# Kernel tuning notes

Measured on AMD Instinct MI355X. Metric: run time of the kernel, lower is better.

Reference implementation:

```python
import jax, jax.numpy as jnp
import numpy as np

T = 2048; H = 1024; NH = 16; NKV = 4; HD = 64
E = 32; TOPK = 4; NG = 4; TG = 2; IM = 384; ISH = 384
ROT = HD // 2          # partial_rotary_factor = 0.5
EPS = 1e-5; RSF = 1.0; THETA = 10000.0


def setup_inputs() -> dict:
    ks = jax.random.split(jax.random.key(0), 12)
    g = lambda k, sh, sc=0.02: jax.random.normal(k, sh, jnp.float32) * sc
    return {
        "hidden_states": g(ks[0], (T, H), 1.0),
        "residual": g(ks[1], (T, H), 1.0),
        "in_ln_w": jnp.ones((H,), jnp.float32),
        "post_ln_w": jnp.ones((H,), jnp.float32),
        "q_norm_w": jnp.ones((HD,), jnp.float32),
        "k_norm_w": jnp.ones((HD,), jnp.float32),
        "Wqkv": g(ks[2], (H, (NH + 2 * NKV) * HD)),
        "Wo": g(ks[3], (NH * HD, H)),
        "Wg": g(ks[4], (H, E)),
        "gate_bias": g(ks[5], (E,), 0.1),
        "Wgu": g(ks[6], (E, H, 2 * IM)),
        "Wd": g(ks[7], (E, IM, H)),
        "Wgu_sh": g(ks[8], (H, 2 * ISH)),
        "Wd_sh": g(ks[9], (ISH, H)),
        "positions": jnp.arange(T, dtype=jnp.int32),
    }


def _rms(x, w):
    return x * jax.lax.rsqrt(jnp.mean(x * x, -1, keepdims=True) + EPS) * w


def _rope(x, pos):
    # neox-style rotary on the first ROT dims of each head; x: [T, nheads, HD]
    half = ROT // 2
    inv = THETA ** (-(jnp.arange(half, dtype=jnp.float32) * 2.0 / ROT))
    ang = pos.astype(jnp.float32)[:, None] * inv          # [T, half]
    c = jnp.cos(ang)[:, None, :]
    s = jnp.sin(ang)[:, None, :]
    x1, x2, rest = x[..., :half], x[..., half:ROT], x[..., ROT:]
    return jnp.concatenate([x1 * c - x2 * s, x1 * s + x2 * c, rest], -1)


def _layer(pos, hidden, residual, in_ln_w, post_ln_w, q_norm_w, k_norm_w,
           Wqkv, Wo, Wg, gate_bias, Wgu, Wd, Wgu_sh, Wd_sh):
    # fused add-RMSNorm (vllm RMSNorm(x, residual))
    residual = hidden + residual
    hidden = _rms(residual, in_ln_w)

    # self-attention (GQA, per-head qk-norm, partial rotary, causal)
    qkv = hidden @ Wqkv
    q = qkv[:, :NH * HD].reshape(T, NH, HD)
    k = qkv[:, NH * HD:(NH + NKV) * HD].reshape(T, NKV, HD)
    v = qkv[:, (NH + NKV) * HD:].reshape(T, NKV, HD)
    q = _rms(q, q_norm_w)
    k = _rms(k, k_norm_w)
    q = _rope(q, pos)
    k = _rope(k, pos)
    rep = NH // NKV
    k = jnp.repeat(k, rep, axis=1)
    v = jnp.repeat(v, rep, axis=1)
    scores = jnp.einsum('thd,shd->hts', q, k) * (HD ** -0.5)
    causal = pos[:, None] >= pos[None, :]
    scores = jnp.where(causal[None], scores, -jnp.inf)
    attn = jax.nn.softmax(scores, axis=-1)
    o = jnp.einsum('hts,shd->thd', attn, v).reshape(T, NH * HD)
    hidden = o @ Wo

    # post-attention fused add-RMSNorm
    residual = hidden + residual
    hidden = _rms(residual, post_ln_w)

    # --- Glm4MoE: grouped sigmoid top-k router with e_score_correction_bias ---
    logits = hidden.astype(jnp.float32) @ Wg            # gate runs in fp32
    scr = jax.nn.sigmoid(logits)                        # [T, E]
    sfc = scr + gate_bias                               # scores_for_choice
    # group score = sum of top-2 biased scores within each group
    gs = jnp.sum(jax.lax.top_k(sfc.reshape(T, NG, E // NG), 2)[0], -1)  # [T, NG]
    _, gidx = jax.lax.top_k(gs, TG)
    gmask = jnp.zeros((T, NG), jnp.float32).at[jnp.arange(T)[:, None], gidx].set(1.0)
    emask = jnp.repeat(gmask, E // NG, axis=1)          # [T, E]
    _, ids = jax.lax.top_k(jnp.where(emask > 0, sfc, -jnp.inf), TOPK)
    w = jnp.take_along_axis(scr, ids, axis=1)           # weights from unbiased scores
    w = w / jnp.sum(w, -1, keepdims=True)               # renormalize (norm_topk_prob)
    wdense = jnp.zeros((T, E), jnp.float32).at[jnp.arange(T)[:, None], ids].set(w)

    # routed experts: dense-over-experts reference for the grouped GEMM dispatch
    gu = jnp.einsum('th,ehi->tei', hidden, Wgu)         # [T, E, 2*IM]
    act = jax.nn.silu(gu[..., :IM]) * gu[..., IM:]      # SiluAndMul
    routed = jnp.einsum('te,tei,eih->th', wdense, act, Wd)

    # shared expert MLP
    gus = hidden @ Wgu_sh
    shared = (jax.nn.silu(gus[:, :ISH]) * gus[:, ISH:]) @ Wd_sh

    hidden = routed * RSF + shared
    return hidden, residual


def reference(hidden_states, residual, in_ln_w, post_ln_w, q_norm_w, k_norm_w,
              Wqkv, Wo, Wg, gate_bias, Wgu, Wd, Wgu_sh, Wd_sh, positions):
    return _layer(positions, hidden_states, residual, in_ln_w, post_ln_w,
                  q_norm_w, k_norm_w, Wqkv, Wo, Wg, gate_bias, Wgu, Wd,
                  Wgu_sh, Wd_sh)
```

## Files before the change

### kernel.cpp

```cpp
#include <hip/hip_runtime.h>
#include <math.h>

#define TT 2048
#define HH 1024
#define NHEADS 16
#define NKVH 4
#define HDIM 64
#define NEXP 32
#define TOPK_ 4
#define NGRP 4
#define IMID 384
#define ISHARED 384
#define QKV_W (24*64)
#define EPS_ 1e-5f
#define MAXSB 288
#define NSPLITS 80

typedef __attribute__((ext_vector_type(8))) short short8;
typedef __attribute__((ext_vector_type(4))) float f32x4;

__device__ __forceinline__ ushort f2bf(float x) {
  union { float f; unsigned u; } v; v.f = x;
  unsigned r = v.u + 0x7fffu + ((v.u >> 16) & 1u);
  return (ushort)(r >> 16);
// ... 12 lines not shown
  return *(const short8*)(As + ((lg * 32 + (row ^ lg)) * 8));
}
__device__ __forceinline__ short8 read_a_frag64(const ushort* As, int lg, int row) {
  return *(const short8*)(As + ((lg * 64 + (row ^ lg)) * 8));
}
__device__ __forceinline__ short8 read_b_frag(const ushort* Bs, int lg, int col) {
  int boff = (col * 16) ^ (((col >> 3) & 7) << 4);
  return *(const short8*)((const char*)Bs + lg * 1024 + boff);
}

__device__ __forceinline__ void stage_B_tile(const float* __restrict__ B, int ldb,
                                             int k0, int col0, ushort* Bs, int tid) {
  int a = tid >> 4;
  int cG = tid & 15;
  int k = 2 * a;
  const float* p0 = B + (size_t)(k0 + k) * ldb + col0 + cG * 4;
  const float* p1 = p0 + ldb;
  float4 r0 = *(const float4*)p0;
  float4 r1 = *(const float4*)p1;
  int gg = (k & 15) >> 2;
  int slot = (k & 3) + ((k >> 4) << 2);
  float v0[4] = {r0.x, r0.y, r0.z, r0.w};
  float v1[4] = {r1.x, r1.y, r1.z, r1.w};
  char* plane = (char*)Bs + gg * 1024;
  #pragma unroll
  for (int j = 0; j < 4; ++j) {
    int c = cG * 4 + j;
    unsigned pk = (unsigned)f2bf(v0[j]) | ((unsigned)f2bf(v1[j]) << 16);
    int boff = ((c * 16) ^ (((c >> 3) & 7) << 4)) + slot * 2;
    *(unsigned*)(plane + boff) = pk;
  }
}

__global__ __launch_bounds__(256) void pack_B_kernel(
    const float* __restrict__ src, ushort* __restrict__ dst, int N) {
  __shared__ ushort tileB[2048];
  int tid = threadIdx.x;
  stage_B_tile(src, N, blockIdx.y * 32, blockIdx.x * 64, tileB, tid);
  __syncthreads();
  size_t toff = ((size_t)blockIdx.y * gridDim.x + blockIdx.x) * 2048;
  *(short8*)(dst + toff + tid * 8) = *(const short8*)(tileB + tid * 8);
}

__global__ __launch_bounds__(256) void gemm64_bb(
    const ushort* __restrict__ Ab, const ushort* __restrict__ Bpk,
    float* __restrict__ C, int M, int N, int K) {
  __shared__ ushort As[4][2048];
  __shared__ ushort Bs[4][2048];
  int tid = threadIdx.x;
  int row0 = blockIdx.y * 64, col0 = blockIdx.x * 64;
  int ntn = N >> 6;
  int wid = tid >> 6, lane = tid & 63;
  int lg = lane >> 4, lr = lane & 15;
  int wrow = (wid >> 1) * 32, wcol = (wid & 1) * 32;
  const ushort* asrc = Ab + (size_t)(row0 + (lane ^ wid)) * K + wid * 8;
  const ushort* bsrc = Bpk + (size_t)blockIdx.x * 2048 + wid * 512 + lane * 8;
  const int NT = K >> 5;
  f32x4 acc[2][2] = {};

  auto issue = [&](int tt) {
    int b = tt & 3;
    gload16(asrc + tt * 32, &As[b][wid * 512]);
    gload16(bsrc + (size_t)tt * ntn * 2048, &Bs[b][wid * 512]);
  };
  issue(0); issue(1); issue(2);
  for (int t = 0; t < NT; ++t) {
    int ahead = NT - 1 - t;
    if (ahead >= 2)      asm volatile("s_waitcnt vmcnt(4)" ::: "memory");
    else if (ahead == 1) asm volatile("s_waitcnt vmcnt(2)" ::: "memory");
    else                 asm volatile("s_waitcnt vmcnt(0)" ::: "memory");
    __builtin_amdgcn_s_barrier();
    if (t + 3 < NT) issue(t + 3);
    int cb = t & 3;
    short8 af0 = read_a_frag64(&As[cb][0], lg, wrow + lr);
    short8 af1 = read_a_frag64(&As[cb][0], lg, wrow + 16 + lr);
    #pragma unroll
    for (int nn = 0; nn < 2; ++nn) {
      short8 bf_ = read_b_frag(&Bs[cb][0], lg, wcol + nn * 16 + lr);
      acc[0][nn] = __builtin_amdgcn_mfma_f32_16x16x32_bf16(af0, bf_, acc[0][nn], 0, 0, 0);
      acc[1][nn] = __builtin_amdgcn_mfma_f32_16x16x32_bf16(af1, bf_, acc[1][nn], 0, 0, 0);
    }
  }
  #pragma unroll
  for (int mm = 0; mm < 2; ++mm)
    #pragma unroll
    for (int nn = 0; nn < 2; ++nn) {
      int row = row0 + wrow + mm * 16 + lg * 4;
      int col = col0 + wcol + nn * 16 + lr;
      #pragma unroll
      for (int i = 0; i < 4; ++i)
        C[(size_t)(row + i) * N + col] = acc[mm][nn][i];
    }
}

__global__ __launch_bounds__(256) void moe_up_pk(
    const ushort* __restrict__ hln2b, const ushort* __restrict__ Wpk,
    const int* __restrict__ perm, const int* __restrict__ offs,
    const int* __restrict__ counts, const int* __restrict__ sb_e,
    const int* __restrict__ sb_base, const int* __restrict__ nsb,
    ushort* __restrict__ actb) {
  int b = blockIdx.x;
  int sb = ((b & 7) * 36) + (b >> 3);
  if (sb >= *nsb) return;
  int e = sb_e[sb];
  int base = sb_base[sb];
  int start = offs[e];
  int nt = min(32, counts[e] - base);
  int tid = threadIdx.x;
  int wid = tid >> 6, lane = tid & 63;
  int lg = lane >> 4, lr = lane & 15;
  int bz = blockIdx.y * 2 + (wid >> 1);
  int wcol = (wid & 1) * 32;
  int tok0 = perm[start + base + min(lr, nt - 1)] >> 2;
  int tok1 = perm[start + base + min(16 + lr, nt - 1)] >> 2;
  const ushort* a0p = hln2b + (size_t)tok0 * HH + lg * 8;
  const ushort* a1p = hln2b + (size_t)tok1 * HH + lg * 8;
  int c0 = wcol + lr, c1 = wcol + 16 + lr;
  int sw0 = (c0 * 16) ^ (((c0 >> 3) & 7) << 4);
  int sw1 = (c1 * 16) ^ (((c1 >> 3) & 7) << 4);
  const char* gbase = (const char*)Wpk + ((size_t)(e * 32) * 12 + bz) * 4096 + lg * 1024;
  const char* ubase = gbase + (size_t)6 * 4096;
  const size_t bstep = (size_t)12 * 4096;
  f32x4 accg[2][2] = {}, accu[2][2] = {};
  short8 a0c = *(const short8*)(a0p);
  short8 a1c = *(const short8*)(a1p);
  short8 g0c = *(const short8*)(gbase + sw0);
  short8 g1c = *(const short8*)(gbase + sw1);
  short8 u0c = *(const short8*)(ubase + sw0);
  short8 u1c = *(const short8*)(ubase + sw1);
  #pragma unroll 4
  for (int t = 0; t < 31; ++t) {
    const char* gb = gbase + (size_t)(t + 1) * bstep;
    const char* ub = ubase + (size_t)(t + 1) * bstep;
    short8 a0n = *(const short8*)(a0p + (t + 1) * 32);
    short8 a1n = *(const short8*)(a1p + (t + 1) * 32);
    short8 g0n = *(const short8*)(gb + sw0);
    short8 g1n = *(const short8*)(gb + sw1);
    short8 u0n = *(const short8*)(ub + sw0);
    short8 u1n = *(const short8*)(ub + sw1);
    accg[0][0] = __builtin_amdgcn_mfma_f32_16x16x32_bf16(a0c, g0c, accg[0][0], 0, 0, 0);
    accg[0][1] = __builtin_amdgcn_mfma_f32_16x16x32_bf16(a0c, g1c, accg[0][1], 0, 0, 0);
    accg[1][0] = __builtin_amdgcn_mfma_f32_16x16x32_bf16(a1c, g0c, accg[1][0], 0, 0, 0);
    accg[1][1] = __builtin_amdgcn_mfma_f32_16x16x32_bf16(a1c, g1c, accg[1][1], 0, 0, 0);
    accu[0][0] = __builtin_amdgcn_mfma_f32_16x16x32_bf16(a0c, u0c, accu[0][0], 0, 0, 0);
    accu[0][1] = __builtin_amdgcn_mfma_f32_16x16x32_bf16(a0c, u1c, accu[0][1], 0, 0, 0);
    accu[1][0] = __builtin_amdgcn_mfma_f32_16x16x32_bf16(a1c, u0c, accu[1][0], 0, 0, 0);
    accu[1][1] = __builtin_amdgcn_mfma_f32_16x16x32_bf16(a1c, u1c, accu[1][1], 0, 0, 0);
    a0c = a0n; a1c = a1n; g0c = g0n; g1c = g1n; u0c = u0n; u1c = u1n;
  }
  accg[0][0] = __builtin_amdgcn_mfma_f32_16x16x32_bf16(a0c, g0c, accg[0][0], 0, 0, 0);
  accg[0][1] = __builtin_amdgcn_mfma_f32_16x16x32_bf16(a0c, g1c, accg[0][1], 0, 0, 0);
  accg[1][0] = __builtin_amdgcn_mfma_f32_16x16x32_bf16(a1c, g0c, accg[1][0], 0, 0, 0);
  accg[1][1] = __builtin_amdgcn_mfma_f32_16x16x32_bf16(a1c, g1c, accg[1][1], 0, 0, 0);
  accu[0][0] = __builtin_amdgcn_mfma_f32_16x16x32_bf16(a0c, u0c, accu[0][0], 0, 0, 0);
  accu[0][1] = __builtin_amdgcn_mfma_f32_16x16x32_bf16(a0c, u1c, accu[0][1], 0, 0, 0);
  accu[1][0] = __builtin_amdgcn_mfma_f32_16x16x32_bf16(a1c, u0c, accu[1][0], 0, 0, 0);
  accu[1][1] = __builtin_amdgcn_mfma_f32_16x16x32_bf16(a1c, u1c, accu[1][1], 0, 0, 0);
  #pragma unroll
  for (int mm = 0; mm < 2; ++mm)
    #pragma unroll
    for (int nn = 0; nn < 2; ++nn) {
      int pcol = bz * 64 + wcol + ((lr >> 2) << 3) + (nn << 2) + (lr & 3);
      #pragma unroll
      for (int i = 0; i < 4; ++i) {
        int rr = mm * 16 + lg * 4 + i;
        if (rr < nt) {
          float gv = accg[mm][nn][i], uv = accu[mm][nn][i];
          float av = gv / (1.f + expf(-gv)) * uv;
          actb[(size_t)(start + base + rr) * IMID + pcol] = f2bf(av);
        }
      }
    }
}

__global__ __launch_bounds__(256) void moe_down_pk(
    const ushort* __restrict__ actb, const ushort* __restrict__ Wpk,
    const int* __restrict__ offs, const int* __restrict__ counts,
    const int* __restrict__ sb_e, const int* __restrict__ sb_base,
    const int* __restrict__ nsb, ushort* __restrict__ partialb) {
  int b = blockIdx.x;
  int sb = ((b & 7) * 36) + (b >> 3);
  if (sb >= *nsb) return;
  int e = sb_e[sb];
  int base = sb_base[sb];
  int start = offs[e];
  int nt = min(32, counts[e] - base);
  __shared__ ushort As[3][1024];
  __shared__ ushort Bs[3][2048];
  int tid = threadIdx.x;
  int bz = blockIdx.y, col0 = bz * 64;
  int wid = tid >> 6, lane = tid & 63;
  int lg = lane >> 4, lr = lane & 15;
  int wrow = (wid >> 1) * 16, wcol = (wid & 1) * 32;
  const ushort* bt0 = Wpk + ((size_t)(e * 12) * 16 + bz) * 2048 + wid * 512 + lane * 8;
  int ga = wid * 2 + (lane >> 5);
  const ushort* asrcA = actb + (size_t)(start + base + ((lane & 31) ^ ga)) * IMID + ga * 8;
  const int NT = IMID >> 5;
  f32x4 acc[2] = {};

  auto issue = [&](int tt) {
    int bb = tt % 3;
    if (wid < 2) gload16(asrcA + tt * 32, &As[bb][wid * 512]);
    gload16(bt0 + (size_t)tt * 16 * 2048, &Bs[bb][wid * 512]);
  };
  issue(0); issue(1);
  for (int t = 0; t < NT; ++t) {
    if (t < NT - 1) {
      if (wid < 2) asm volatile("s_waitcnt vmcnt(2)" ::: "memory");
      else         asm volatile("s_waitcnt vmcnt(1)" ::: "memory");
    } else {
      asm volatile("s_waitcnt vmcnt(0)" ::: "memory");
    }
    __builtin_amdgcn_s_barrier();
    if (t + 2 < NT) issue(t + 2);
    int cb = t % 3;
    short8 af = read_a_frag32(&As[cb][0], lg, wrow + lr);
    #pragma unroll
    for (int nn = 0; nn < 2; ++nn) {
      short8 bf_ = read_b_frag(&Bs[cb][0], lg, wcol + nn * 16 + lr);
      acc[nn] = __builtin_amdgcn_mfma_f32_16x16x32_bf16(af, bf_, acc[nn], 0, 0, 0);
    }
  }
  #pragma unroll
  for (int nn = 0; nn < 2; ++nn)
    #pragma unroll
    for (int i = 0; i < 4; ++i) {
      int rr = wrow + lg * 4 + i;
      if (rr < nt)
        partialb[(size_t)(start + base + rr) * HH + col0 + wcol + nn * 16 + lr] = f2bf(acc[nn][i]);
    }
}

__global__ __launch_bounds__(256) void add_rms_kernel(
    const float* __restrict__ a, const float* __restrict__ b,
    const float* __restrict__ w, float* __restrict__ sum_out,
    float* __restrict__ ln_out, ushort* __restrict__ lnb) {
  int t = blockIdx.x, tid = threadIdx.x;
  float4 x = reinterpret_cast<const float4*>(a + (size_t)t*HH)[tid];
  float4 y = reinterpret_cast<const float4*>(b + (size_t)t*HH)[tid];
  x.x += y.x; x.y += y.y; x.z += y.z; x.w += y.w;
  float ss = x.x*x.x + x.y*x.y + x.z*x.z + x.w*x.w;
  #pragma unroll
  for (int off = 1; off < 64; off <<= 1) ss += __shfl_xor(ss, off);
  __shared__ float wsum[4];
  int wid = tid >> 6, lane = tid & 63;
  if (lane == 0) wsum[wid] = ss;
  __syncthreads();
  float tot = wsum[0] + wsum[1] + wsum[2] + wsum[3];
  float r = rsqrtf(tot * (1.0f/HH) + EPS_);
  reinterpret_cast<float4*>(sum_out + (size_t)t*HH)[tid] = x;
  float4 wl = reinterpret_cast<const float4*>(w)[tid];
  float4 o = make_float4(x.x*r*wl.x, x.y*r*wl.y, x.z*r*wl.z, x.w*r*wl.w);
  reinterpret_cast<float4*>(ln_out + (size_t)t*HH)[tid] = o;
  ushort4 ub;
  ub.x = f2bf(o.x); ub.y = f2bf(o.y); ub.z = f2bf(o.z); ub.w = f2bf(o.w);
  int dst = ((tid >> 3) << 5) + ((tid & 3) << 3) + (((tid >> 2) & 1) << 2);
  *(ushort4*)(lnb + (size_t)t * HH + dst) = ub;
}

__global__ __launch_bounds__(256) void qk_norm_rope_kernel(
    float* __restrict__ qkv, const float* __restrict__ qw,
    const float* __restrict__ kw, const int* __restrict__ pos) {
  int t = blockIdx.x;
  int hh = blockIdx.y * 4 + (threadIdx.x >> 6);
  int lane = threadIdx.x & 63;
  float* p = qkv + (size_t)t * QKV_W + hh * HDIM;
  float x = p[lane];
  float ss = x * x;
  #pragma unroll
  for (int off = 1; off < 64; off <<= 1) ss += __shfl_xor(ss, off);
  float r = rsqrtf(ss * (1.0f/HDIM) + EPS_);
  float wv = (hh < NHEADS ? qw : kw)[lane];
  float xn = x * r * wv;
  float partner = __shfl_xor(xn, 16);
  float out = xn;
  if (lane < 32) {
    int i = lane & 15;
    float inv = powf(10000.0f, -(float)i / 16.0f);
    float ang = (float)pos[t] * inv;
    float cv = cosf(ang), sv = sinf(ang);
    out = (lane < 16) ? (xn * cv - partner * sv) : (partner * sv + xn * cv);
  }
  p[lane] = out;
}

__global__ __launch_bounds__(256) void pack_KV_kernel(
    const float* __restrict__ qkv, ushort* __restrict__ Kpk,
    ushort* __restrict__ Vpk) {
  __shared__ ushort kimg[2048];
  __shared__ ushort vimg[2048];
  int tid = threadIdx.x;
  int kt = blockIdx.x, kvh = blockIdx.y;
  {
    int c = tid >> 7, t2 = tid & 127;
    int g = t2 & 3, r = t2 >> 2;
    const float* kp = qkv + (size_t)(kt*32 + r) * QKV_W + NHEADS*HDIM + kvh*HDIM + 32*c + 4*g;
    float4 h0 = *(const float4*)kp;
    float4 h1 = *(const float4*)(kp + 16);
    short8 v;
    v[0]=(short)f2bf(h0.x); v[1]=(short)f2bf(h0.y); v[2]=(short)f2bf(h0.z); v[3]=(short)f2bf(h0.w);
    v[4]=(short)f2bf(h1.x); v[5]=(short)f2bf(h1.y); v[6]=(short)f2bf(h1.z); v[7]=(short)f2bf(h1.w);
    *(short8*)(kimg + c*1024 + (g*32 + (r^g))*8) = v;
  }
  stage_B_tile(qkv + (size_t)(NHEADS+NKVH)*HDIM + (size_t)kvh*HDIM, QKV_W, kt*32, 0, vimg, tid);
  __syncthreads();
  size_t toff = ((size_t)(kvh * (TT/32) + kt)) * 2048;
  *(short8*)(Kpk + toff + tid * 8) = *(const short8*)(kimg + tid * 8);
  *(short8*)(Vpk + toff + tid * 8) = *(const short8*)(vimg + tid * 8);
}

__global__ __launch_bounds__(256) void attn_v3_kernel(
    const float* __restrict__ qkv, const ushort* __restrict__ Kpk,
    const ushort* __restrict__ Vpk, ushort* __restrict__ ob,
    float* __restrict__ po, float* __restrict__ pl) {
  __shared__ ushort Ks[3][2048];
  __shared__ ushort Vs[3][2048];
  int tid = threadIdx.x;
  int wid = tid >> 6, lane = tid & 63;
  int lg = lane >> 4, lr = lane & 15;
  int h = blockIdx.y;
  int f = blockIdx.x;
  int g = 0;
  while (f >= 4 * (g + 1) * (g + 2)) ++g;
  int r_ = f - 4 * g * (g + 1);
  int ns = g + 1;
  int qb = 8 * g + r_ / ns;
  int s = r_ % ns;
  int tiles_total = 2 * qb + 2;
  int per = (tiles_total + ns - 1) / ns;
  int lo = s * per;
  int nloc = min(per, tiles_total - lo);
  int kvh = h >> 2;
  int q0 = qb * 64 + wid * 16;
  int qg = q0 + lr;
  const float SCL = 0.125f * 1.44269504f;
  const float FM = 16.0f;

  const float* qrow = qkv + (size_t)qg * QKV_W + h * HDIM;
  short8 qfr[2];
  #pragma unroll
  for (int c = 0; c < 2; ++c) {
    float4 a = *(const float4*)(qrow + 32*c + 4*lg);
    float4 b = *(const float4*)(qrow + 32*c + 4*lg + 16);
    short8 v;
    v[0]=(short)f2bf(a.x*SCL); v[1]=(short)f2bf(a.y*SCL); v[2]=(short)f2bf(a.z*SCL); v[3]=(short)f2bf(a.w*SCL);
    v[4]=(short)f2bf(b.x*SCL); v[5]=(short)f2bf(b.y*SCL); v[6]=(short)f2bf(b.z*SCL); v[7]=(short)f2bf(b.w*SCL);
    qfr[c] = v;
  }

  const ushort* ksrc = Kpk + (size_t)(kvh * (TT/32) + lo) * 2048 + wid * 512 + lane * 8;
  const ushort* vsrc = Vpk + (size_t)(kvh * (TT/32) + lo) * 2048 + wid * 512 + lane * 8;

  f32x4 o_acc[4] = {};
  float l_st = 0.f;
// ... 53 lines not shown
    short8 pa = pu.s8;
    #pragma unroll
    for (int nd = 0; nd < 4; ++nd) {
      short8 vf = read_b_frag(&Vs[cb][0], lg, 16*nd + lr);
      o_acc[nd] = __builtin_amdgcn_mfma_f32_16x16x32_bf16(pa, vf, o_acc[nd], 0, 0, 0);
    }
  }

  if (ns == 1) {
    #pragma unroll
    for (int i = 0; i < 4; ++i) {
      float lrow = __shfl(l_st, 4*lg + i);
      float inv = 1.0f / lrow;
      int row = q0 + 4*lg + i;
      ushort* op = ob + (size_t)row * (NHEADS*HDIM) + h * HDIM;
      #pragma unroll
      for (int nd = 0; nd < 4; ++nd) {
        int pcol = ((nd >> 1) << 5) + ((lr >> 2) << 3) + ((nd & 1) << 2) + (lr & 3);
        op[pcol] = f2bf(o_acc[nd][i] * inv);
      }
    }
  } else {
    float* pob = po + ((size_t)f * NHEADS + h) * 4096;
    #pragma unroll
    for (int nd = 0; nd < 4; ++nd)
      #pragma unroll
      for (int i = 0; i < 4; ++i)
        pob[(wid * 16 + lg * 4 + i) * 64 + 16 * nd + lr] = o_acc[nd][i];
    if (lg == 0)
      pl[((size_t)f * NHEADS + h) * 64 + wid * 16 + lr] = l_st;
  }
}

__global__ __launch_bounds__(256) void attn_combine_kernel(
    const float* __restrict__ po, const float* __restrict__ pl,
    ushort* __restrict__ ob) {
  int h = blockIdx.x;
  int qb = 8 + blockIdx.y;
  int g = qb >> 3;
  int ns = g + 1;
  int f0 = 4 * g * (g + 1) + (qb - 8 * g) * ns;
  int tid = threadIdx.x;
  int r = tid >> 2, c = tid & 3;
  float acc[16] = {};
  float lsum = 0.f;
  for (int s = 0; s < ns; ++s) {
    size_t base = ((size_t)(f0 + s) * NHEADS + h) * 4096 + r * 64 + c * 16;
    #pragma unroll
    for (int j = 0; j < 4; ++j) {
      float4 v = *(const float4*)(po + base + j * 4);
      acc[j*4+0] += v.x; acc[j*4+1] += v.y; acc[j*4+2] += v.z; acc[j*4+3] += v.w;
    }
    lsum += pl[((size_t)(f0 + s) * NHEADS + h) * 64 + r];
  }
  float inv = 1.0f / lsum;
  int row = qb * 64 + r;
  ushort* op = ob + (size_t)row * (NHEADS*HDIM) + h * HDIM + (c >> 1) * 32 + (c & 1) * 4;
  #pragma unroll
  for (int a = 0; a < 4; ++a) {
    ushort4 u;
    u.x = f2bf(acc[a*4+0] * inv); u.y = f2bf(acc[a*4+1] * inv);
    u.z = f2bf(acc[a*4+2] * inv); u.w = f2bf(acc[a*4+3] * inv);
    *(ushort4*)(op + a * 8) = u;
  }
}

__global__ __launch_bounds__(256) void router_kernel(
    const float* __restrict__ hln, const float* __restrict__ Wg,
    const float* __restrict__ bias, int* __restrict__ sel_e,
    float* __restrict__ sel_w) {
  __shared__ float hid[4][HH];
  int tid = threadIdx.x, wid = tid >> 6, lane = tid & 63;
  int t = blockIdx.x * 4 + wid;
  const float4* src = (const float4*)(hln + (size_t)t * HH);
  float4* dst = (float4*)hid[wid];
  #pragma unroll
  for (int j = 0; j < 4; ++j) dst[j * 64 + lane] = src[j * 64 + lane];
  int e = lane & 31, half = lane >> 5;
  const float* wp = Wg + (size_t)(half * 512) * NEXP + e;
  const float* hp = hid[wid] + half * 512;
  float p = 0.f;
  #pragma unroll 8
  for (int h = 0; h < 512; ++h) p += hp[h] * wp[(size_t)h * NEXP];
  p += __shfl_xor(p, 32);
  float sc = 1.0f / (1.0f + expf(-p));
  float sfc = sc + bias[e];
  float m1 = sfc, m2 = -1e30f;
  #pragma unroll
  for (int off = 1; off <= 4; off <<= 1) {
    float om1 = __shfl_xor(m1, off), om2 = __shfl_xor(m2, off);
    float hi_ = fmaxf(m1, om1);
    float lo_ = fmaxf(fminf(m1, om1), fmaxf(m2, om2));
    m1 = hi_; m2 = lo_;
  }
  float gs = m1 + m2;
  float gv[4] = {__shfl(gs, 0), __shfl(gs, 8), __shfl(gs, 16), __shfl(gs, 24)};
  int g1 = 0; float b1 = gv[0];
  #pragma unroll
  for (int g = 1; g < 4; ++g) if (gv[g] > b1) { b1 = gv[g]; g1 = g; }
  int g2 = -1; float b2 = -1e30f;
  #pragma unroll
  for (int g = 0; g < 4; ++g) if (g != g1 && gv[g] > b2) { b2 = gv[g]; g2 = g; }
  bool keep = ((e >> 3) == g1) || ((e >> 3) == g2);
  float cand = keep ? sfc : -1e30f;
  int ids[4]; float wv[4]; float wsum = 0.f;
  #pragma unroll
  for (int s = 0; s < 4; ++s) {
    float v = cand; int ix = e;
    #pragma unroll
    for (int off = 1; off < 64; off <<= 1) {
      float ov = __shfl_xor(v, off); int oix = __shfl_xor(ix, off);
      if (ov > v || (ov == v && oix < ix)) { v = ov; ix = oix; }
    }
    ids[s] = ix;
    if (e == ix) cand = -1e30f;
    float w = __shfl(sc, ix);
    wv[s] = w; wsum += w;
  }
  if (lane == 0) {
    #pragma unroll
    for (int s = 0; s < 4; ++s) {
      sel_e[t * 4 + s] = ids[s];
      sel_w[t * 4 + s] = wv[s] / wsum;
    }
  }
}

__global__ __launch_bounds__(256) void count_kernel(
    const int* __restrict__ sel_e, int* __restrict__ counts) {
  int e = blockIdx.x, tid = threadIdx.x;
  int c = 0;
  for (int i = tid; i < TT * TOPK_; i += 256) c += (sel_e[i] == e);
  #pragma unroll
  for (int off = 1; off < 64; off <<= 1) c += __shfl_xor(c, off);
  __shared__ int wsum[4];
  if ((tid & 63) == 0) wsum[tid >> 6] = c;
  __syncthreads();
  if (tid == 0) counts[e] = wsum[0] + wsum[1] + wsum[2] + wsum[3];
}

__global__ void scan_kernel(const int* __restrict__ counts,
                            int* __restrict__ offs, int* __restrict__ cursor,
                            int* __restrict__ sb_e, int* __restrict__ sb_base,
                            int* __restrict__ nsb) {
  if (threadIdx.x == 0) {
    int acc = 0, n = 0;
    for (int e = 0; e < NEXP; ++e) {
      offs[e] = acc; cursor[e] = acc;
      int c = counts[e];
      for (int b = 0; b < c; b += 32) { sb_e[n] = e; sb_base[n] = b; ++n; }
      acc += c;
    }
    *nsb = n;
  }
}

__global__ void scatter_kernel(const int* __restrict__ sel_e,
                               int* __restrict__ cursor, int* __restrict__ perm,
                               int* __restrict__ ipos) {
  int i = blockIdx.x * 256 + threadIdx.x;
  if (i < TT * TOPK_) {
    int e = sel_e[i];
    int pos = atomicAdd(&cursor[e], 1);
    perm[pos] = i;
    ipos[i] = pos;
  }
}

__global__ __launch_bounds__(256) void silu_shared_kernel(
    const float* __restrict__ gus, ushort* __restrict__ shsb) {
  int i = blockIdx.x * 256 + threadIdx.x;
  if (i < TT * (ISHARED/4)) {
    int t = i / (ISHARED/4), k = i % (ISHARED/4);
    const float* gp = gus + (size_t)t * (2*ISHARED) + k * 4;
    float4 g4 = *(const float4*)gp;
    float4 u4 = *(const float4*)(gp + ISHARED);
    ushort4 r;
    r.x = f2bf(g4.x / (1.f + expf(-g4.x)) * u4.x);
    r.y = f2bf(g4.y / (1.f + expf(-g4.y)) * u4.y);
    r.z = f2bf(g4.z / (1.f + expf(-g4.z)) * u4.z);
    r.w = f2bf(g4.w / (1.f + expf(-g4.w)) * u4.w);
    int pdst = ((k >> 3) << 5) + ((k & 3) << 3) + (((k >> 2) & 1) << 2);
// ... 46 lines not shown
  float* R_A   = f + off; off += (size_t)TT*HH;
  float* HLN   = f + off; off += (size_t)TT*HH;
  float* QKV   = f + off; off += (size_t)TT*QKV_W;
  float* OATT  = f + off; off += (size_t)TT*HH;
  float* HLN2  = f + off; off += (size_t)TT*HH;
  float* SELW  = f + off; off += (size_t)TT*TOPK_;
  float* PO    = f + off; off += (size_t)NSPLITS*NHEADS*4096;
  float* PL    = f + off; off += (size_t)NSPLITS*NHEADS*64;
  ushort* HLNB  = (ushort*)(f + off); off += (size_t)TT*HH/2;
  ushort* HLN2B = (ushort*)(f + off); off += (size_t)TT*HH/2;
  ushort* OATTB = (ushort*)(f + off); off += (size_t)TT*HH/2;
  ushort* SHSB  = (ushort*)(f + off); off += (size_t)TT*ISHARED/2;
  ushort* KPK   = (ushort*)(f + off); off += (size_t)NKVH*(TT/32)*2048/2;
  ushort* VPK   = (ushort*)(f + off); off += (size_t)NKVH*(TT/32)*2048/2;
  ushort* ACTB  = (ushort*)(f + off); off += (size_t)(TT*TOPK_ + 128)*IMID/2;
  ushort* PARTB = (ushort*)(f + off); off += (size_t)TT*TOPK_*HH/2;
  ushort* PK_QKV = (ushort*)(f + off); off += (size_t)HH*QKV_W/2;
  ushort* PK_WO  = (ushort*)(f + off); off += (size_t)HH*HH/2;
  ushort* PK_WGU = (ushort*)(f + off); off += (size_t)NEXP*HH*(2*IMID)/2;
  ushort* PK_WD  = (ushort*)(f + off); off += (size_t)NEXP*IMID*HH/2;
  ushort* PK_GUSH= (ushort*)(f + off); off += (size_t)HH*(2*ISHARED)/2;
  ushort* PK_DSH = (ushort*)(f + off); off += (size_t)ISHARED*HH/2;
  int* ibase   = (int*)(f + off);
  int* SELE    = ibase;
  int* PERM    = ibase + TT*TOPK_;
  int* IPOS    = ibase + 2*TT*TOPK_;
  int* COUNTS  = ibase + 3*TT*TOPK_;
  int* OFFS    = COUNTS + NEXP;
  int* CURSOR  = OFFS + NEXP;
  int* SB_E    = CURSOR + NEXP;
  int* SB_BASE = SB_E + MAXSB;
  int* NSB     = SB_BASE + MAXSB;

  pack_B_kernel<<<dim3(QKV_W/64, HH/32), 256, 0, stream>>>(Wqkv, PK_QKV, QKV_W);
  pack_B_kernel<<<dim3(HH/64, HH/32), 256, 0, stream>>>(Wo, PK_WO, HH);
  pack_B_kernel<<<dim3((2*IMID)/64, NEXP*HH/32), 256, 0, stream>>>(Wgu, PK_WGU, 2*IMID);
  pack_B_kernel<<<dim3(HH/64, NEXP*IMID/32), 256, 0, stream>>>(Wd, PK_WD, HH);
  pack_B_kernel<<<dim3((2*ISHARED)/64, HH/32), 256, 0, stream>>>(Wgu_sh, PK_GUSH, 2*ISHARED);
  pack_B_kernel<<<dim3(HH/64, ISHARED/32), 256, 0, stream>>>(Wd_sh, PK_DSH, HH);

  add_rms_kernel<<<TT, 256, 0, stream>>>(hidden, residual, in_ln_w, R_A, HLN, HLNB);
  gemm64_bb<<<dim3(QKV_W/64, TT/64), 256, 0, stream>>>(HLNB, PK_QKV, QKV, TT, QKV_W, HH);
  qk_norm_rope_kernel<<<dim3(TT, 5), 256, 0, stream>>>(QKV, q_norm_w, k_norm_w, positions);
  pack_KV_kernel<<<dim3(TT/32, NKVH), 256, 0, stream>>>(QKV, KPK, VPK);
  attn_v3_kernel<<<dim3(NSPLITS, NHEADS), 256, 0, stream>>>(QKV, KPK, VPK, OATTB, PO, PL);
  attn_combine_kernel<<<dim3(NHEADS, 24), 256, 0, stream>>>(PO, PL, OATTB);
  gemm64_bb<<<dim3(HH/64, TT/64), 256, 0, stream>>>(OATTB, PK_WO, HLN, TT, HH, HH);
  add_rms_kernel<<<TT, 256, 0, stream>>>(HLN, R_A, post_ln_w, out + (size_t)TT*HH, HLN2, HLN2B);
  router_kernel<<<TT/4, 256, 0, stream>>>(HLN2, Wg, gate_bias, SELE, SELW);
  count_kernel<<<NEXP, 256, 0, stream>>>(SELE, COUNTS);
  scan_kernel<<<1, 64, 0, stream>>>(COUNTS, OFFS, CURSOR, SB_E, SB_BASE, NSB);
  scatter_kernel<<<(TT*TOPK_ + 255)/256, 256, 0, stream>>>(SELE, CURSOR, PERM, IPOS);
  moe_up_pk<<<dim3(MAXSB, 3), 256, 0, stream>>>(HLN2B, PK_WGU, PERM, OFFS, COUNTS, SB_E, SB_BASE, NSB, ACTB);
  moe_down_pk<<<dim3(MAXSB, HH/64), 256, 0, stream>>>(ACTB, PK_WD, OFFS, COUNTS, SB_E, SB_BASE, NSB, PARTB);
  gemm64_bb<<<dim3((2*ISHARED)/64, TT/64), 256, 0, stream>>>(HLN2B, PK_GUSH, QKV, TT, 2*ISHARED, HH);
  silu_shared_kernel<<<(TT*(ISHARED/4) + 255)/256, 256, 0, stream>>>(QKV, SHSB);
  gemm64_bb<<<dim3(HH/64, TT/64), 256, 0, stream>>>(SHSB, PK_DSH, OATT, TT, HH, ISHARED);
  final_combine_kernel<<<TT, 256, 0, stream>>>(PARTB, SELW, IPOS, OATT, out);
}
```

Measured before the change: 341.9 us.

## Merge independent kernels into horizontally fused launches to overlap work

Independent kernels are combined into single launches that dispatch on block index. The weight packing and the first add-RMSNorm share one launch. Expert weight packing runs alongside attention. The shared-expert GEMMs run alongside the routed MoE up and down GEMMs, and count and scan are merged into one kernel using shared-memory atomics. The aim is to cut launch overhead and fill idle CUs during small or imbalanced phases. In exchange, the fused kernels take on the largest shared-memory footprint of their branches, which can lower occupancy.

```diff
diff --git a/kernel.cpp b/kernel.cpp
--- a/kernel.cpp
+++ b/kernel.cpp
@@ -68,29 +68,54 @@
   }
 }
 
-__global__ __launch_bounds__(256) void pack_B_kernel(
-    const float* __restrict__ src, ushort* __restrict__ dst, int N) {
-  __shared__ ushort tileB[2048];
+__device__ __forceinline__ void pack_B_body(
+    const float* __restrict__ src, ushort* __restrict__ dst, int N,
+    int ntn, int kt, int nt, ushort* tileB, int tid) {
+  stage_B_tile(src, N, kt * 32, nt * 64, tileB, tid);
+  __syncthreads();
+  size_t toff = ((size_t)kt * ntn + nt) * 2048;
+  *(short8*)(dst + toff + tid * 8) = *(const short8*)(tileB + tid * 8);
+}
+
+__device__ __forceinline__ void add_rms_body(
+    const float* __restrict__ a, const float* __restrict__ b,
+    const float* __restrict__ w, float* __restrict__ sum_out,
+    float* __restrict__ ln_out, ushort* __restrict__ lnb,
+    int t, int tid, float* wsum) {
+  float4 x = reinterpret_cast<const float4*>(a + (size_t)t*HH)[tid];
+  float4 y = reinterpret_cast<const float4*>(b + (size_t)t*HH)[tid];
+  x.x += y.x; x.y += y.y; x.z += y.z; x.w += y.w;
+  float ss = x.x*x.x + x.y*x.y + x.z*x.z + x.w*x.w;
+  #pragma unroll
+  for (int off = 1; off < 64; off <<= 1) ss += __shfl_xor(ss, off);
+  int wid = tid >> 6, lane = tid & 63;
+  if (lane == 0) wsum[wid] = ss;
+  __syncthreads();
+  float tot = wsum[0] + wsum[1] + wsum[2] + wsum[3];
+  float r = rsqrtf(tot * (1.0f/HH) + EPS_);
+  reinterpret_cast<float4*>(sum_out + (size_t)t*HH)[tid] = x;
+  float4 wl = reinterpret_cast<const float4*>(w)[tid];
+  float4 o = make_float4(x.x*r*wl.x, x.y*r*wl.y, x.z*r*wl.z, x.w*r*wl.w);
+  reinterpret_cast<float4*>(ln_out + (size_t)t*HH)[tid] = o;
+  ushort4 ub;
+  ub.x = f2bf(o.x); ub.y = f2bf(o.y); ub.z = f2bf(o.z); ub.w = f2bf(o.w);
+  int dst = ((tid >> 3) << 5) + ((tid & 3) << 3) + (((tid >> 2) & 1) << 2);
+  *(ushort4*)(lnb + (size_t)t * HH + dst) = ub;
+}
+
+__device__ __forceinline__ void gemm64_body(
+    const ushort* __restrict__ Ab, const ushort* __restrict__ Bpk,
+    float* __restrict__ C, int M, int N, int K, int bx, int by, char* smem) {
+  ushort (*As)[2048] = (ushort(*)[2048])smem;
+  ushort (*Bs)[2048] = (ushort(*)[2048])(smem + 16384);
   int tid = threadIdx.x;
-  stage_B_tile(src, N, blockIdx.y * 32, blockIdx.x * 64, tileB, tid);
-  __syncthreads();
-  size_t toff = ((size_t)blockIdx.y * gridDim.x + blockIdx.x) * 2048;
-  *(short8*)(dst + toff + tid * 8) = *(const short8*)(tileB + tid * 8);
-}
-
-__global__ __launch_bounds__(256) void gemm64_bb(
-    const ushort* __restrict__ Ab, const ushort* __restrict__ Bpk,
-    float* __restrict__ C, int M, int N, int K) {
-  __shared__ ushort As[4][2048];
-  __shared__ ushort Bs[4][2048];
-  int tid = threadIdx.x;
-  int row0 = blockIdx.y * 64, col0 = blockIdx.x * 64;
+  int row0 = by * 64, col0 = bx * 64;
   int ntn = N >> 6;
   int wid = tid >> 6, lane = tid & 63;
   int lg = lane >> 4, lr = lane & 15;
   int wrow = (wid >> 1) * 32, wcol = (wid & 1) * 32;
   const ushort* asrc = Ab + (size_t)(row0 + (lane ^ wid)) * K + wid * 8;
-  const ushort* bsrc = Bpk + (size_t)blockIdx.x * 2048 + wid * 512 + lane * 8;
+  const ushort* bsrc = Bpk + (size_t)bx * 2048 + wid * 512 + lane * 8;
   const int NT = K >> 5;
   f32x4 acc[2][2] = {};
 
@@ -129,13 +154,19 @@
     }
 }
 
-__global__ __launch_bounds__(256) void moe_up_pk(
+__global__ __launch_bounds__(256) void gemm64_bb(
+    const ushort* __restrict__ Ab, const ushort* __restrict__ Bpk,
+    float* __restrict__ C, int M, int N, int K) {
+  __shared__ char smem[32768];
+  gemm64_body(Ab, Bpk, C, M, N, K, blockIdx.x, blockIdx.y, smem);
+}
+
+__device__ __forceinline__ void moe_up_body(
     const ushort* __restrict__ hln2b, const ushort* __restrict__ Wpk,
     const int* __restrict__ perm, const int* __restrict__ offs,
     const int* __restrict__ counts, const int* __restrict__ sb_e,
     const int* __restrict__ sb_base, const int* __restrict__ nsb,
-    ushort* __restrict__ actb) {
-  int b = blockIdx.x;
+    ushort* __restrict__ actb, int b, int by) {
   int sb = ((b & 7) * 36) + (b >> 3);
   if (sb >= *nsb) return;
   int e = sb_e[sb];
@@ -145,7 +176,7 @@
   int tid = threadIdx.x;
   int wid = tid >> 6, lane = tid & 63;
   int lg = lane >> 4, lr = lane & 15;
-  int bz = blockIdx.y * 2 + (wid >> 1);
+  int bz = by * 2 + (wid >> 1);
   int wcol = (wid & 1) * 32;
   int tok0 = perm[start + base + min(lr, nt - 1)] >> 2;
   int tok1 = perm[start + base + min(16 + lr, nt - 1)] >> 2;
@@ -209,22 +240,22 @@
     }
 }
 
-__global__ __launch_bounds__(256) void moe_down_pk(
+__device__ __forceinline__ void moe_down_body(
     const ushort* __restrict__ actb, const ushort* __restrict__ Wpk,
     const int* __restrict__ offs, const int* __restrict__ counts,
     const int* __restrict__ sb_e, const int* __restrict__ sb_base,
-    const int* __restrict__ nsb, ushort* __restrict__ partialb) {
-  int b = blockIdx.x;
+    const int* __restrict__ nsb, ushort* __restrict__ partialb,
+    int b, int bz, char* smem) {
   int sb = ((b & 7) * 36) + (b >> 3);
   if (sb >= *nsb) return;
+  ushort (*As)[1024] = (ushort(*)[1024])smem;
+  ushort (*Bs)[2048] = (ushort(*)[2048])(smem + 6144);
   int e = sb_e[sb];
   int base = sb_base[sb];
   int start = offs[e];
   int nt = min(32, counts[e] - base);
-  __shared__ ushort As[3][1024];
-  __shared__ ushort Bs[3][2048];
   int tid = threadIdx.x;
-  int bz = blockIdx.y, col0 = bz * 64;
+  int col0 = bz * 64;
   int wid = tid >> 6, lane = tid & 63;
   int lg = lane >> 4, lr = lane & 15;
   int wrow = (wid >> 1) * 16, wcol = (wid & 1) * 32;
@@ -267,95 +298,15 @@
     }
 }
 
-__global__ __launch_bounds__(256) void add_rms_kernel(
-    const float* __restrict__ a, const float* __restrict__ b,
-    const float* __restrict__ w, float* __restrict__ sum_out,
-    float* __restrict__ ln_out, ushort* __restrict__ lnb) {
-  int t = blockIdx.x, tid = threadIdx.x;
-  float4 x = reinterpret_cast<const float4*>(a + (size_t)t*HH)[tid];
-  float4 y = reinterpret_cast<const float4*>(b + (size_t)t*HH)[tid];
-  x.x += y.x; x.y += y.y; x.z += y.z; x.w += y.w;
-  float ss = x.x*x.x + x.y*x.y + x.z*x.z + x.w*x.w;
-  #pragma unroll
-  for (int off = 1; off < 64; off <<= 1) ss += __shfl_xor(ss, off);
-  __shared__ float wsum[4];
-  int wid = tid >> 6, lane = tid & 63;
-  if (lane == 0) wsum[wid] = ss;
-  __syncthreads();
-  float tot = wsum[0] + wsum[1] + wsum[2] + wsum[3];
-  float r = rsqrtf(tot * (1.0f/HH) + EPS_);
-  reinterpret_cast<float4*>(sum_out + (size_t)t*HH)[tid] = x;
-  float4 wl = reinterpret_cast<const float4*>(w)[tid];
-  float4 o = make_float4(x.x*r*wl.x, x.y*r*wl.y, x.z*r*wl.z, x.w*r*wl.w);
-  reinterpret_cast<float4*>(ln_out + (size_t)t*HH)[tid] = o;
-  ushort4 ub;
-  ub.x = f2bf(o.x); ub.y = f2bf(o.y); ub.z = f2bf(o.z); ub.w = f2bf(o.w);
-  int dst = ((tid >> 3) << 5) + ((tid & 3) << 3) + (((tid >> 2) & 1) << 2);
-  *(ushort4*)(lnb + (size_t)t * HH + dst) = ub;
-}
-
-__global__ __launch_bounds__(256) void qk_norm_rope_kernel(
-    float* __restrict__ qkv, const float* __restrict__ qw,
-    const float* __restrict__ kw, const int* __restrict__ pos) {
-  int t = blockIdx.x;
-  int hh = blockIdx.y * 4 + (threadIdx.x >> 6);
-  int lane = threadIdx.x & 63;
-  float* p = qkv + (size_t)t * QKV_W + hh * HDIM;
-  float x = p[lane];
-  float ss = x * x;
-  #pragma unroll
-  for (int off = 1; off < 64; off <<= 1) ss += __shfl_xor(ss, off);
-  float r = rsqrtf(ss * (1.0f/HDIM) + EPS_);
-  float wv = (hh < NHEADS ? qw : kw)[lane];
-  float xn = x * r * wv;
-  float partner = __shfl_xor(xn, 16);
-  float out = xn;
-  if (lane < 32) {
-    int i = lane & 15;
-    float inv = powf(10000.0f, -(float)i / 16.0f);
-    float ang = (float)pos[t] * inv;
-    float cv = cosf(ang), sv = sinf(ang);
-    out = (lane < 16) ? (xn * cv - partner * sv) : (partner * sv + xn * cv);
-  }
-  p[lane] = out;
-}
-
-__global__ __launch_bounds__(256) void pack_KV_kernel(
-    const float* __restrict__ qkv, ushort* __restrict__ Kpk,
-    ushort* __restrict__ Vpk) {
-  __shared__ ushort kimg[2048];
-  __shared__ ushort vimg[2048];
-  int tid = threadIdx.x;
-  int kt = blockIdx.x, kvh = blockIdx.y;
-  {
-    int c = tid >> 7, t2 = tid & 127;
-    int g = t2 & 3, r = t2 >> 2;
-    const float* kp = qkv + (size_t)(kt*32 + r) * QKV_W + NHEADS*HDIM + kvh*HDIM + 32*c + 4*g;
-    float4 h0 = *(const float4*)kp;
-    float4 h1 = *(const float4*)(kp + 16);
-    short8 v;
-    v[0]=(short)f2bf(h0.x); v[1]=(short)f2bf(h0.y); v[2]=(short)f2bf(h0.z); v[3]=(short)f2bf(h0.w);
-    v[4]=(short)f2bf(h1.x); v[5]=(short)f2bf(h1.y); v[6]=(short)f2bf(h1.z); v[7]=(short)f2bf(h1.w);
-    *(short8*)(kimg + c*1024 + (g*32 + (r^g))*8) = v;
-  }
-  stage_B_tile(qkv + (size_t)(NHEADS+NKVH)*HDIM + (size_t)kvh*HDIM, QKV_W, kt*32, 0, vimg, tid);
-  __syncthreads();
-  size_t toff = ((size_t)(kvh * (TT/32) + kt)) * 2048;
-  *(short8*)(Kpk + toff + tid * 8) = *(const short8*)(kimg + tid * 8);
-  *(short8*)(Vpk + toff + tid * 8) = *(const short8*)(vimg + tid * 8);
-}
-
-__global__ __launch_bounds__(256) void attn_v3_kernel(
+__device__ __forceinline__ void attn_body(
     const float* __restrict__ qkv, const ushort* __restrict__ Kpk,
     const ushort* __restrict__ Vpk, ushort* __restrict__ ob,
-    float* __restrict__ po, float* __restrict__ pl) {
-  __shared__ ushort Ks[3][2048];
-  __shared__ ushort Vs[3][2048];
+    float* __restrict__ po, float* __restrict__ pl, int f, int h, char* smem) {
+  ushort (*Ks)[2048] = (ushort(*)[2048])smem;
+  ushort (*Vs)[2048] = (ushort(*)[2048])(smem + 12288);
   int tid = threadIdx.x;
   int wid = tid >> 6, lane = tid & 63;
   int lg = lane >> 4, lr = lane & 15;
-  int h = blockIdx.y;
-  int f = blockIdx.x;
   int g = 0;
   while (f >= 4 * (g + 1) * (g + 2)) ++g;
   int r_ = f - 4 * g * (g + 1);
@@ -475,6 +426,139 @@
   }
 }
 
+__global__ __launch_bounds__(256) void fused_prep_kernel(
+    const float* __restrict__ hidden, const float* __restrict__ residual,
+    const float* __restrict__ in_ln_w, float* __restrict__ R_A,
+    float* __restrict__ HLN, ushort* __restrict__ HLNB,
+    const float* __restrict__ Wqkv, ushort* __restrict__ PK_QKV,
+    const float* __restrict__ Wo, ushort* __restrict__ PK_WO,
+    const float* __restrict__ Wgu_sh, ushort* __restrict__ PK_GUSH,
+    const float* __restrict__ Wd_sh, ushort* __restrict__ PK_DSH) {
+  __shared__ ushort smem[2048];
+  int blk = blockIdx.x, tid = threadIdx.x;
+  if (blk < 2048) {
+    add_rms_body(hidden, residual, in_ln_w, R_A, HLN, HLNB, blk, tid, (float*)smem);
+  } else if (blk < 2816) {
+    int q = blk - 2048;
+    pack_B_body(Wqkv, PK_QKV, QKV_W, 24, q / 24, q % 24, smem, tid);
+  } else if (blk < 3328) {
+    int q = blk - 2816;
+    pack_B_body(Wo, PK_WO, HH, 16, q / 16, q % 16, smem, tid);
+  } else if (blk < 3712) {
+    int q = blk - 3328;
+    pack_B_body(Wgu_sh, PK_GUSH, 2*ISHARED, 12, q / 12, q % 12, smem, tid);
+  } else {
+    int q = blk - 3712;
+    pack_B_body(Wd_sh, PK_DSH, HH, 16, q / 16, q % 16, smem, tid);
+  }
+}
+
+__global__ __launch_bounds__(256) void fused_attn_kernel(
+    const float* __restrict__ qkv, const ushort* __restrict__ Kpk,
+    const ushort* __restrict__ Vpk, ushort* __restrict__ ob,
+    float* __restrict__ po, float* __restrict__ pl,
+    const float* __restrict__ Wgu, ushort* __restrict__ PK_WGU,
+    const float* __restrict__ Wd, ushort* __restrict__ PK_WD) {
+  __shared__ char smem[24576];
+  int blk = blockIdx.x, tid = threadIdx.x;
+  if (blk < 1280) {
+    attn_body(qkv, Kpk, Vpk, ob, po, pl, blk % NSPLITS, blk / NSPLITS, smem);
+  } else if (blk < 13568) {
+    int q = blk - 1280;
+    pack_B_body(Wgu, PK_WGU, 2*IMID, 12, q / 12, q % 12, (ushort*)smem, tid);
+  } else {
+    int q = blk - 13568;
+    pack_B_body(Wd, PK_WD, HH, 16, q / 16, q % 16, (ushort*)smem, tid);
+  }
+}
+
+__global__ __launch_bounds__(256) void fused_up_kernel(
+    const ushort* __restrict__ hln2b, const ushort* __restrict__ PK_WGU,
+    const int* __restrict__ perm, const int* __restrict__ offs,
+    const int* __restrict__ counts, const int* __restrict__ sb_e,
+    const int* __restrict__ sb_base, const int* __restrict__ nsb,
+    ushort* __restrict__ actb,
+    const ushort* __restrict__ PK_GUSH, float* __restrict__ gus_out) {
+  __shared__ char smem[32768];
+  int blk = blockIdx.x;
+  if (blk < 384) {
+    gemm64_body(hln2b, PK_GUSH, gus_out, TT, 2*ISHARED, HH, blk % 12, blk / 12, smem);
+  } else {
+    int q = blk - 384;
+    moe_up_body(hln2b, PK_WGU, perm, offs, counts, sb_e, sb_base, nsb, actb,
+                q % MAXSB, q / MAXSB);
+  }
+}
+
+__global__ __launch_bounds__(256) void fused_down_kernel(
+    const ushort* __restrict__ actb, const ushort* __restrict__ PK_WD,
+    const int* __restrict__ offs, const int* __restrict__ counts,
+    const int* __restrict__ sb_e, const int* __restrict__ sb_base,
+    const int* __restrict__ nsb, ushort* __restrict__ partialb,
+    const ushort* __restrict__ shsb, const ushort* __restrict__ PK_DSH,
+    float* __restrict__ shared_out) {
+  __shared__ char smem[32768];
+  int blk = blockIdx.x;
+  if (blk < 512) {
+    gemm64_body(shsb, PK_DSH, shared_out, TT, HH, ISHARED, blk % 16, blk / 16, smem);
+  } else {
+    int q = blk - 512;
+    moe_down_body(actb, PK_WD, offs, counts, sb_e, sb_base, nsb, partialb,
+                  q % MAXSB, q / MAXSB, smem);
+  }
+}
+
+__global__ __launch_bounds__(256) void qk_norm_rope_kernel(
+    float* __restrict__ qkv, const float* __restrict__ qw,
+    const float* __restrict__ kw, const int* __restrict__ pos) {
+  int t = blockIdx.x;
+  int hh = blockIdx.y * 4 + (threadIdx.x >> 6);
+  int lane = threadIdx.x & 63;
+  float* p = qkv + (size_t)t * QKV_W + hh * HDIM;
+  float x = p[lane];
+  float ss = x * x;
+  #pragma unroll
+  for (int off = 1; off < 64; off <<= 1) ss += __shfl_xor(ss, off);
+  float r = rsqrtf(ss * (1.0f/HDIM) + EPS_);
+  float wv = (hh < NHEADS ? qw : kw)[lane];
+  float xn = x * r * wv;
+  float partner = __shfl_xor(xn, 16);
+  float out = xn;
+  if (lane < 32) {
+    int i = lane & 15;
+    float inv = powf(10000.0f, -(float)i / 16.0f);
+    float ang = (float)pos[t] * inv;
+    float cv = cosf(ang), sv = sinf(ang);
+    out = (lane < 16) ? (xn * cv - partner * sv) : (partner * sv + xn * cv);
+  }
+  p[lane] = out;
+}
+
+__global__ __launch_bounds__(256) void pack_KV_kernel(
+    const float* __restrict__ qkv, ushort* __restrict__ Kpk,
+    ushort* __restrict__ Vpk) {
+  __shared__ ushort kimg[2048];
+  __shared__ ushort vimg[2048];
+  int tid = threadIdx.x;
+  int kt = blockIdx.x, kvh = blockIdx.y;
+  {
+    int c = tid >> 7, t2 = tid & 127;
+    int g = t2 & 3, r = t2 >> 2;
+    const float* kp = qkv + (size_t)(kt*32 + r) * QKV_W + NHEADS*HDIM + kvh*HDIM + 32*c + 4*g;
+    float4 h0 = *(const float4*)kp;
+    float4 h1 = *(const float4*)(kp + 16);
+    short8 v;
+    v[0]=(short)f2bf(h0.x); v[1]=(short)f2bf(h0.y); v[2]=(short)f2bf(h0.z); v[3]=(short)f2bf(h0.w);
+    v[4]=(short)f2bf(h1.x); v[5]=(short)f2bf(h1.y); v[6]=(short)f2bf(h1.z); v[7]=(short)f2bf(h1.w);
+    *(short8*)(kimg + c*1024 + (g*32 + (r^g))*8) = v;
+  }
+  stage_B_tile(qkv + (size_t)(NHEADS+NKVH)*HDIM + (size_t)kvh*HDIM, QKV_W, kt*32, 0, vimg, tid);
+  __syncthreads();
+  size_t toff = ((size_t)(kvh * (TT/32) + kt)) * 2048;
+  *(short8*)(Kpk + toff + tid * 8) = *(const short8*)(kimg + tid * 8);
+  *(short8*)(Vpk + toff + tid * 8) = *(const short8*)(vimg + tid * 8);
+}
+
 __global__ __launch_bounds__(256) void attn_combine_kernel(
     const float* __restrict__ po, const float* __restrict__ pl,
     ushort* __restrict__ ob) {
@@ -508,6 +592,14 @@
   }
 }
 
+__global__ __launch_bounds__(256) void add_rms_kernel(
+    const float* __restrict__ a, const float* __restrict__ b,
+    const float* __restrict__ w, float* __restrict__ sum_out,
+    float* __restrict__ ln_out, ushort* __restrict__ lnb) {
+  __shared__ float wsum[4];
+  add_rms_body(a, b, w, sum_out, ln_out, lnb, blockIdx.x, threadIdx.x, wsum);
+}
+
 __global__ __launch_bounds__(256) void router_kernel(
     const float* __restrict__ hln, const float* __restrict__ Wg,
     const float* __restrict__ bias, int* __restrict__ sel_e,
@@ -569,28 +661,22 @@
   }
 }
 
-__global__ __launch_bounds__(256) void count_kernel(
-    const int* __restrict__ sel_e, int* __restrict__ counts) {
-  int e = blockIdx.x, tid = threadIdx.x;
-  int c = 0;
-  for (int i = tid; i < TT * TOPK_; i += 256) c += (sel_e[i] == e);
-  #pragma unroll
-  for (int off = 1; off < 64; off <<= 1) c += __shfl_xor(c, off);
-  __shared__ int wsum[4];
-  if ((tid & 63) == 0) wsum[tid >> 6] = c;
+__global__ __launch_bounds__(256) void count_scan_kernel(
+    const int* __restrict__ sel_e, int* __restrict__ counts,
+    int* __restrict__ offs, int* __restrict__ cursor,
+    int* __restrict__ sb_e, int* __restrict__ sb_base, int* __restrict__ nsb) {
+  __shared__ int cnt[NEXP];
+  int tid = threadIdx.x;
+  if (tid < NEXP) cnt[tid] = 0;
   __syncthreads();
-  if (tid == 0) counts[e] = wsum[0] + wsum[1] + wsum[2] + wsum[3];
-}
-
-__global__ void scan_kernel(const int* __restrict__ counts,
-                            int* __restrict__ offs, int* __restrict__ cursor,
-                            int* __restrict__ sb_e, int* __restrict__ sb_base,
-                            int* __restrict__ nsb) {
-  if (threadIdx.x == 0) {
+  for (int i = tid; i < TT * TOPK_; i += 256) atomicAdd(&cnt[sel_e[i]], 1);
+  __syncthreads();
+  if (tid == 0) {
     int acc = 0, n = 0;
     for (int e = 0; e < NEXP; ++e) {
+      int c = cnt[e];
+      counts[e] = c;
       offs[e] = acc; cursor[e] = acc;
-      int c = counts[e];
       for (int b = 0; b < c; b += 32) { sb_e[n] = e; sb_base[n] = b; ++n; }
       acc += c;
     }
@@ -703,29 +789,24 @@
   int* SB_BASE = SB_E + MAXSB;
   int* NSB     = SB_BASE + MAXSB;
 
-  pack_B_kernel<<<dim3(QKV_W/64, HH/32), 256, 0, stream>>>(Wqkv, PK_QKV, QKV_W);
-  pack_B_kernel<<<dim3(HH/64, HH/32), 256, 0, stream>>>(Wo, PK_WO, HH);
-  pack_B_kernel<<<dim3((2*IMID)/64, NEXP*HH/32), 256, 0, stream>>>(Wgu, PK_WGU, 2*IMID);
-  pack_B_kernel<<<dim3(HH/64, NEXP*IMID/32), 256, 0, stream>>>(Wd, PK_WD, HH);
-  pack_B_kernel<<<dim3((2*ISHARED)/64, HH/32), 256, 0, stream>>>(Wgu_sh, PK_GUSH, 2*ISHARED);
-  pack_B_kernel<<<dim3(HH/64, ISHARED/32), 256, 0, stream>>>(Wd_sh, PK_DSH, HH);
-
-  add_rms_kernel<<<TT, 256, 0, stream>>>(hidden, residual, in_ln_w, R_A, HLN, HLNB);
+  fused_prep_kernel<<<3904, 256, 0, stream>>>(
+      hidden, residual, in_ln_w, R_A, HLN, HLNB,
+      Wqkv, PK_QKV, Wo, PK_WO, Wgu_sh, PK_GUSH, Wd_sh, PK_DSH);
   gemm64_bb<<<dim3(QKV_W/64, TT/64), 256, 0, stream>>>(HLNB, PK_QKV, QKV, TT, QKV_W, HH);
   qk_norm_rope_kernel<<<dim3(TT, 5), 256, 0, stream>>>(QKV, q_norm_w, k_norm_w, positions);
   pack_KV_kernel<<<dim3(TT/32, NKVH), 256, 0, stream>>>(QKV, KPK, VPK);
-  attn_v3_kernel<<<dim3(NSPLITS, NHEADS), 256, 0, stream>>>(QKV, KPK, VPK, OATTB, PO, PL);
+  fused_attn_kernel<<<19712, 256, 0, stream>>>(QKV, KPK, VPK, OATTB, PO, PL,
+                                               Wgu, PK_WGU, Wd, PK_WD);
   attn_combine_kernel<<<dim3(NHEADS, 24), 256, 0, stream>>>(PO, PL, OATTB);
   gemm64_bb<<<dim3(HH/64, TT/64), 256, 0, stream>>>(OATTB, PK_WO, HLN, TT, HH, HH);
   add_rms_kernel<<<TT, 256, 0, stream>>>(HLN, R_A, post_ln_w, out + (size_t)TT*HH, HLN2, HLN2B);
   router_kernel<<<TT/4, 256, 0, stream>>>(HLN2, Wg, gate_bias, SELE, SELW);
-  count_kernel<<<NEXP, 256, 0, stream>>>(SELE, COUNTS);
-  scan_kernel<<<1, 64, 0, stream>>>(COUNTS, OFFS, CURSOR, SB_E, SB_BASE, NSB);
+  count_scan_kernel<<<1, 256, 0, stream>>>(SELE, COUNTS, OFFS, CURSOR, SB_E, SB_BASE, NSB);
   scatter_kernel<<<(TT*TOPK_ + 255)/256, 256, 0, stream>>>(SELE, CURSOR, PERM, IPOS);
-  moe_up_pk<<<dim3(MAXSB, 3), 256, 0, stream>>>(HLN2B, PK_WGU, PERM, OFFS, COUNTS, SB_E, SB_BASE, NSB, ACTB);
-  moe_down_pk<<<dim3(MAXSB, HH/64), 256, 0, stream>>>(ACTB, PK_WD, OFFS, COUNTS, SB_E, SB_BASE, NSB, PARTB);
-  gemm64_bb<<<dim3((2*ISHARED)/64, TT/64), 256, 0, stream>>>(HLN2B, PK_GUSH, QKV, TT, 2*ISHARED, HH);
+  fused_up_kernel<<<384 + MAXSB*3, 256, 0, stream>>>(
+      HLN2B, PK_WGU, PERM, OFFS, COUNTS, SB_E, SB_BASE, NSB, ACTB, PK_GUSH, QKV);
   silu_shared_kernel<<<(TT*(ISHARED/4) + 255)/256, 256, 0, stream>>>(QKV, SHSB);
-  gemm64_bb<<<dim3(HH/64, TT/64), 256, 0, stream>>>(SHSB, PK_DSH, OATT, TT, HH, ISHARED);
+  fused_down_kernel<<<512 + MAXSB*(HH/64), 256, 0, stream>>>(
+      ACTB, PK_WD, OFFS, COUNTS, SB_E, SB_BASE, NSB, PARTB, SHSB, PK_DSH, OATT);
   final_combine_kernel<<<TT, 256, 0, stream>>>(PARTB, SELW, IPOS, OATT, out);
 }
```

New measurement: 299.4 us. 1.14x faster.
